# Optimization experiments

Hardware: AMD Instinct MI355X
Metric: run time of the kernel (lower is better)

## Reference

```python
import jax, jax.numpy as jnp
import numpy as np
import math

B, T, S = 32, 512, 256          # batch, tgt_len (prediction_length), src_len (encoder tokens)
PD, ED = 1, 768                 # pred_dim, encoder_dim
D, H, L, FF = 256, 8, 4, 1024   # d_model, nhead, num_layers, dim_feedforward
HD = D // H
NEG = -1e9
EPS = 1e-5


def _pos_encoding(seq_len, d_model):
    pos = jnp.arange(seq_len, dtype=jnp.float32)[:, None]
    div = jnp.exp(jnp.arange(0, d_model, 2, dtype=jnp.float32) * (-math.log(10000.0) / d_model))
    pe = jnp.zeros((seq_len, d_model), jnp.float32)
    pe = pe.at[:, 0::2].set(jnp.sin(pos * div))
    pe = pe.at[:, 1::2].set(jnp.cos(pos * div))
    return pe


def _ln(x, g, b):
    m = jnp.mean(x, -1, keepdims=True)
    v = jnp.mean((x - m) ** 2, -1, keepdims=True)
    return (x - m) * jax.lax.rsqrt(v + EPS) * g + b


def _mha(xq, xkv, Wq, bq, Wk, bk, Wv, bv, Wo, bo, mask):
    b, t, d = xq.shape
    s = xkv.shape[1]
    Q = (xq @ Wq + bq).reshape(b, t, H, HD).transpose(0, 2, 1, 3)   # bhtd
    K = (xkv @ Wk + bk).reshape(b, s, H, HD).transpose(0, 2, 1, 3)  # bhsd
    V = (xkv @ Wv + bv).reshape(b, s, H, HD).transpose(0, 2, 1, 3)
    scores = jnp.einsum('bhtd,bhsd->bhts', Q, K) * (HD ** -0.5)
    if mask is not None:
        scores = scores + mask
    w = jax.nn.softmax(scores, axis=-1)
    o = jnp.einsum('bhts,bhsd->bhtd', w, V).transpose(0, 2, 1, 3).reshape(b, t, d)
    return o @ Wo + bo


def _forward(tgt, memory, W_emb, b_emb, W_enc, b_enc,
             Wq_s, bq_s, Wk_s, bk_s, Wv_s, bv_s, Wo_s, bo_s,
             Wq_c, bq_c, Wk_c, bk_c, Wv_c, bv_c, Wo_c, bo_c,
             g1, be1, g2, be2, g3, be3, Wf1, bf1, Wf2, bf2,
             Wp1, bp1, Wp2, bp2):
    t = tgt.shape[1]
    x = tgt @ W_emb + b_emb + _pos_encoding(t, D)          # (B,T,D)
    mem = memory @ W_enc + b_enc                           # (B,S,D)
    causal = jnp.triu(jnp.full((t, t), NEG, jnp.float32), k=1)
    for i in range(L):
        sa = _mha(x, x, Wq_s[i], bq_s[i], Wk_s[i], bk_s[i], Wv_s[i], bv_s[i], Wo_s[i], bo_s[i], causal)
        x = _ln(x + sa, g1[i], be1[i])
        ca = _mha(x, mem, Wq_c[i], bq_c[i], Wk_c[i], bk_c[i], Wv_c[i], bv_c[i], Wo_c[i], bo_c[i], None)
        x = _ln(x + ca, g2[i], be2[i])
        ff = jax.nn.gelu(x @ Wf1[i] + bf1[i], approximate=False) @ Wf2[i] + bf2[i]
        x = _ln(x + ff, g3[i], be3[i])
    h = jax.nn.gelu(x @ Wp1 + bp1, approximate=False)
    return h @ Wp2 + bp2                                   # (B,T,PD)


def setup_inputs() -> dict:
    key = jax.random.key(0)
    keys = iter(jax.random.split(key, 40))
    def rn(shape, scale=0.05):
        return jax.random.normal(next(keys), shape, jnp.float32) * scale
    z = jnp.zeros
    inp = {
        'tgt': jax.random.normal(next(keys), (B, T, PD), jnp.float32),
        'memory': jax.random.normal(next(keys), (B, S, ED), jnp.float32),
        'W_emb': rn((PD, D)), 'b_emb': z((D,)),
        'W_enc': rn((ED, D)), 'b_enc': z((D,)),
        'Wq_s': rn((L, D, D)), 'bq_s': z((L, D)),
        'Wk_s': rn((L, D, D)), 'bk_s': z((L, D)),
        'Wv_s': rn((L, D, D)), 'bv_s': z((L, D)),
        'Wo_s': rn((L, D, D)), 'bo_s': z((L, D)),
        'Wq_c': rn((L, D, D)), 'bq_c': z((L, D)),
        'Wk_c': rn((L, D, D)), 'bk_c': z((L, D)),
        'Wv_c': rn((L, D, D)), 'bv_c': z((L, D)),
        'Wo_c': rn((L, D, D)), 'bo_c': z((L, D)),
        'g1': jnp.ones((L, D)), 'be1': z((L, D)),
        'g2': jnp.ones((L, D)), 'be2': z((L, D)),
        'g3': jnp.ones((L, D)), 'be3': z((L, D)),
        'Wf1': rn((L, D, FF)), 'bf1': z((L, FF)),
        'Wf2': rn((L, FF, D)), 'bf2': z((L, D)),
        'Wp1': rn((D, D // 2)), 'bp1': z((D // 2,)),
        'Wp2': rn((D // 2, PD), 0.01), 'bp2': jnp.full((PD,), 0.1, jnp.float32),
    }
    return inp


def reference(tgt, memory, W_emb, b_emb, W_enc, b_enc,
              Wq_s, bq_s, Wk_s, bk_s, Wv_s, bv_s, Wo_s, bo_s,
              Wq_c, bq_c, Wk_c, bk_c, Wv_c, bv_c, Wo_c, bo_c,
              g1, be1, g2, be2, g3, be3, Wf1, bf1, Wf2, bf2,
              Wp1, bp1, Wp2, bp2):
    return _forward(tgt, memory, W_emb, b_emb, W_enc, b_enc,
                    Wq_s, bq_s, Wk_s, bk_s, Wv_s, bv_s, Wo_s, bo_s,
                    Wq_c, bq_c, Wk_c, bk_c, Wv_c, bv_c, Wo_c, bo_c,
                    g1, be1, g2, be2, g3, be3, Wf1, bf1, Wf2, bf2,
                    Wp1, bp1, Wp2, bp2)
```

## Files before the change

kernel.cpp:

```cpp
#include <hip/hip_runtime.h>
#include <math.h>

#define B_  32
#define T_  512
#define S_  256
#define D_  256
#define H_  8
#define HD_ 32
#define FF_ 1024
#define ED_ 768
#define L_  4
#define BT_ (B_*T_)
#define BS_ (B_*S_)

typedef __bf16 bf16x8_t __attribute__((ext_vector_type(8)));
typedef __bf16 bf16x4_t __attribute__((ext_vector_type(4)));
typedef float  f32x4_t  __attribute__((ext_vector_type(4)));

__device__ __forceinline__ float gelu_f(float v) {
  return 0.5f * v * (1.f + erff(v * 0.7071067811865476f));
}

__device__ __forceinline__ void gl16(const __bf16* gsrc, __bf16* ldst) {
  __builtin_amdgcn_global_load_lds(
      (const __attribute__((address_space(1))) unsigned int*)gsrc,
      (__attribute__((address_space(3))) unsigned int*)ldst, 16, 0, 0);
}

__global__ __launch_bounds__(256)
void embed_kernel(const float* __restrict__ tgt, const float* __restrict__ Wemb,
                  const float* __restrict__ bemb, float* __restrict__ x,
                  __bf16* __restrict__ xbf) {
  int i = blockIdx.x * 256 + threadIdx.x;
  int d  = i & (D_ - 1);
  int bt = i >> 8;
  int t  = bt & (T_ - 1);
  int p  = d >> 1;
  float div = expf((float)(2 * p) * (-9.210340371976184f / (float)D_));
  float arg = (float)t * div;
  float pe = (d & 1) ? cosf(arg) : sinf(arg);
  float v = tgt[bt] * Wemb[d] + bemb[d] + pe;
  x[i] = v;
  xbf[i] = (__bf16)v;
}

__global__ __launch_bounds__(256)
void cvt_bf16_kernel(const float* __restrict__ in, __bf16* __restrict__ out) {
  int i = (blockIdx.x * 256 + threadIdx.x) * 4;
  float4 v = *(const float4*)(in + i);
  bf16x4_t o;
  o[0] = (__bf16)v.x; o[1] = (__bf16)v.y; o[2] = (__bf16)v.z; o[3] = (__bf16)v.w;
  *(bf16x4_t*)(out + i) = o;
}

struct TD { const float* src; size_t dst; int K, N, nb; size_t lstride; };
struct TDs { TD d[12]; };

__global__ __launch_bounds__(256)
void transpose_cvt_kernel(TDs a, __bf16* __restrict__ wt) {
  __shared__ float tile[32][33];
  TD t = a.d[blockIdx.y];
  const int kt = t.K >> 5, nt = t.N >> 5;
  const int per = kt * nt, tot = per * t.nb;
  const int id = blockIdx.x;
  if (id >= tot) return;
  const int b = id / per;
  const int r2 = id - b * per;
  const int kti = r2 / nt;
  const int nti = r2 - kti * nt;
  const int c = threadIdx.x & 31, r0 = threadIdx.x >> 5;
  const float* src = t.src + (size_t)b * t.K * t.N;
  __bf16* dst = wt + t.dst + (size_t)b * t.lstride;
#pragma unroll
  for (int j = 0; j < 4; ++j) {
    int rr = r0 + j * 8;
    tile[rr][c] = src[(size_t)(kti * 32 + rr) * t.N + nti * 32 + c];
  }
  __syncthreads();
#pragma unroll
  for (int j = 0; j < 4; ++j) {
    int rr = r0 + j * 8;
    dst[(size_t)(nti * 32 + rr) * t.K + kti * 32 + c] = (__bf16)tile[c][rr];
  }
}

__global__ __launch_bounds__(256)
void bias_concat_kernel(const float* __restrict__ bq_s, const float* __restrict__ bk_s,
                        const float* __restrict__ bv_s, const float* __restrict__ bk_c,
                        const float* __restrict__ bv_c, float* __restrict__ dst) {
  int idx = blockIdx.x * 256 + threadIdx.x;
  if (idx >= 5120) return;
  if (idx < 3072) {
    int l = idx / 768, c = idx - l * 768;
    float v = (c < 256) ? bq_s[l * 256 + c]
            : (c < 512) ? bk_s[l * 256 + c - 256]
                        : bv_s[l * 256 + c - 512];
    dst[idx] = v;
  } else {
    int j = idx - 3072;
    int l = j / 512, c = j - l * 512;
    float v = (c < 256) ? bk_c[l * 256 + c] : bv_c[l * 256 + c - 256];
    dst[idx] = v;
  }
}

template<int ACT, int OBF>
__global__ __launch_bounds__(256, 3)
void gemm_bf(const __bf16* __restrict__ A, const __bf16* __restrict__ Bt,
             const float* __restrict__ bias, void* __restrict__ Cv,
             int N, int K, int nN, int ppx) {
  __shared__ __bf16 As[128 * 64];
  __shared__ __bf16 Bs[64 * 64];
  const int tid = threadIdx.x, lane = tid & 63, wv = tid >> 6;
  const int wm = (wv & 1) * 64, wn = (wv >> 1) * 32;
  const int ln15 = lane & 15, kgrp = lane >> 4;
  const int xcd = blockIdx.x & 7, j = blockIdx.x >> 3;
  const int bm = (xcd * ppx + j / nN) * 128;
  const int bn = (j % nN) * 64;

  const int r8 = lane >> 3;
  const int scol = (lane & 7) ^ r8;
  const __bf16* a_g = A  + (size_t)(bm + wv * 32 + r8) * K + scol * 8;
  const __bf16* b_g = Bt + (size_t)(bn + wv * 16 + r8) * K + scol * 8;
  __bf16* a_l = As + wv * 2048;
  __bf16* b_l = Bs + wv * 1024;

  const int xk0 = kgrp ^ (ln15 & 7);
  const int xk1 = (4 + kgrp) ^ (ln15 & 7);

  f32x4_t acc[4][2];
#pragma unroll
  for (int mi = 0; mi < 4; ++mi)
#pragma unroll
    for (int ni = 0; ni < 2; ++ni) acc[mi][ni] = (f32x4_t){0.f, 0.f, 0.f, 0.f};

  for (int k0 = 0; k0 < K; k0 += 64) {
    gl16(a_g + k0,                a_l);
    gl16(a_g + k0 + (size_t)8*K,  a_l + 512);
    gl16(a_g + k0 + (size_t)16*K, a_l + 1024);
    gl16(a_g + k0 + (size_t)24*K, a_l + 1536);
    gl16(b_g + k0,                b_l);
    gl16(b_g + k0 + (size_t)8*K,  b_l + 512);
    __syncthreads();

#pragma unroll
    for (int kk = 0; kk < 2; ++kk) {
      const int xk = kk ? xk1 : xk0;
      bf16x8_t b0 = *(const bf16x8_t*)(Bs + ((wn + ln15) * 8 + xk) * 8);
      bf16x8_t b1 = *(const bf16x8_t*)(Bs + ((wn + 16 + ln15) * 8 + xk) * 8);
#pragma unroll
      for (int mi = 0; mi < 4; ++mi) {
        bf16x8_t af = *(const bf16x8_t*)(As + ((wm + mi * 16 + ln15) * 8 + xk) * 8);
        acc[mi][0] = __builtin_amdgcn_mfma_f32_16x16x32_bf16(af, b0, acc[mi][0], 0, 0, 0);
        acc[mi][1] = __builtin_amdgcn_mfma_f32_16x16x32_bf16(af, b1, acc[mi][1], 0, 0, 0);
      }
    }
    __syncthreads();
  }

#pragma unroll
  for (int mi = 0; mi < 4; ++mi) {
#pragma unroll
    for (int ni = 0; ni < 2; ++ni) {
      const int ocol = bn + wn + ni * 16 + ln15;
      const float bv = bias[ocol];
      const int orow0 = bm + wm + mi * 16 + kgrp * 4;
#pragma unroll
      for (int r = 0; r < 4; ++r) {
        float o = acc[mi][ni][r] + bv;
        if (ACT == 1) o = gelu_f(o);
        if (OBF) ((__bf16*)Cv)[(size_t)(orow0 + r) * N + ocol] = (__bf16)o;
        else     ((float*)Cv)[(size_t)(orow0 + r) * N + ocol] = o;
      }
    }
  }
}

template<int ACT, int OBF>
__global__ __launch_bounds__(256, 3)
void gemm_bf2(const __bf16* __restrict__ A, const __bf16* __restrict__ Bt,
              const float* __restrict__ bias, void* __restrict__ Cv,
              int N, int K, int nN, int ppx) {
  __shared__ __bf16 As[128 * 64];
  __shared__ __bf16 Bs[128 * 64];
  const int tid = threadIdx.x, lane = tid & 63, wv = tid >> 6;
  const int wm = (wv & 1) * 64, wn = (wv >> 1) * 64;
  const int ln15 = lane & 15, kgrp = lane >> 4;
  const int xcd = blockIdx.x & 7, j = blockIdx.x >> 3;
  const int bm = (xcd * ppx + j / nN) * 128;
  const int bn = (j % nN) * 128;

  const int r8 = lane >> 3;
  const int scol = (lane & 7) ^ r8;
  const __bf16* a_g = A  + (size_t)(bm + wv * 32 + r8) * K + scol * 8;
  const __bf16* b_g = Bt + (size_t)(bn + wv * 32 + r8) * K + scol * 8;
  __bf16* a_l = As + wv * 2048;
  __bf16* b_l = Bs + wv * 2048;

  const int xk0 = kgrp ^ (ln15 & 7);
  const int xk1 = (4 + kgrp) ^ (ln15 & 7);

  f32x4_t acc[4][4];
#pragma unroll
  for (int mi = 0; mi < 4; ++mi)
#pragma unroll
    for (int ni = 0; ni < 4; ++ni) acc[mi][ni] = (f32x4_t){0.f, 0.f, 0.f, 0.f};

  for (int k0 = 0; k0 < K; k0 += 64) {
    gl16(a_g + k0,                a_l);
    gl16(a_g + k0 + (size_t)8*K,  a_l + 512);
    gl16(a_g + k0 + (size_t)16*K, a_l + 1024);
    gl16(a_g + k0 + (size_t)24*K, a_l + 1536);
    gl16(b_g + k0,                b_l);
    gl16(b_g + k0 + (size_t)8*K,  b_l + 512);
    gl16(b_g + k0 + (size_t)16*K, b_l + 1024);
    gl16(b_g + k0 + (size_t)24*K, b_l + 1536);
    __syncthreads();

#pragma unroll
    for (int kk = 0; kk < 2; ++kk) {
      const int xk = kk ? xk1 : xk0;
      bf16x8_t bfr[4];
#pragma unroll
      for (int ni = 0; ni < 4; ++ni)
        bfr[ni] = *(const bf16x8_t*)(Bs + ((wn + ni * 16 + ln15) * 8 + xk) * 8);
#pragma unroll
      for (int mi = 0; mi < 4; ++mi) {
        bf16x8_t af = *(const bf16x8_t*)(As + ((wm + mi * 16 + ln15) * 8 + xk) * 8);
#pragma unroll
        for (int ni = 0; ni < 4; ++ni)
          acc[mi][ni] = __builtin_amdgcn_mfma_f32_16x16x32_bf16(af, bfr[ni], acc[mi][ni], 0, 0, 0);
      }
    }
    __syncthreads();
  }

#pragma unroll
  for (int mi = 0; mi < 4; ++mi) {
#pragma unroll
    for (int ni = 0; ni < 4; ++ni) {
      const int ocol = bn + wn + ni * 16 + ln15;
      const float bv = bias[ocol];
      const int orow0 = bm + wm + mi * 16 + kgrp * 4;
#pragma unroll
      for (int r = 0; r < 4; ++r) {
        float o = acc[mi][ni][r] + bv;
        if (ACT == 1) o = gelu_f(o);
        if (OBF) ((__bf16*)Cv)[(size_t)(orow0 + r) * N + ocol] = (__bf16)o;
        else     ((float*)Cv)[(size_t)(orow0 + r) * N + ocol] = o;
      }
    }
  }
}

template<bool CAUSAL>
__global__ __launch_bounds__(256)
void attn_mfma(const __bf16* __restrict__ Q, const __bf16* __restrict__ K,
               const __bf16* __restrict__ V, __bf16* __restrict__ O,
               int KVROWS, int qs, int ks) {
  const int b = blockIdx.x >> 3, h = blockIdx.x & 7;
  const int qt = blockIdx.y;
  const int tid = threadIdx.x, lane = tid & 63, wv = tid >> 6;
  const int ln15 = lane & 15, kgrp = lane >> 4, kgrp8 = kgrp * 8;

  __shared__ __bf16 K_lds[64][36];
  __shared__ __bf16 Vt_lds[32][72];
  __shared__ __bf16 P_lds[4][16][72];

  const int q_glob = qt * 64 + wv * 16 + ln15;
  const bf16x8_t qfrag = *(const bf16x8_t*)(Q + (size_t)(b * T_ + q_glob) * qs + h * HD_ + kgrp8);

  const int s_r = tid >> 2, s_c8 = (tid & 3) * 8;
  const __bf16* Kb = K + (size_t)(b * KVROWS + s_r) * ks + h * HD_ + s_c8;
  const __bf16* Vb = V + (size_t)(b * KVROWS + s_r) * ks + h * HD_ + s_c8;

  f32x4_t o0 = (f32x4_t){0.f,0.f,0.f,0.f}, o1 = (f32x4_t){0.f,0.f,0.f,0.f};
  float m = -3.0e38f, l = 0.f;
  const float SCALE = 0.17677669529663689f;
  const int slim = CAUSAL ? (qt + 1) * 64 : KVROWS;

  for (int s0 = 0; s0 < slim; s0 += 64) {
    *(bf16x8_t*)&K_lds[s_r][s_c8] = *(const bf16x8_t*)(Kb + (size_t)s0 * ks);
    bf16x8_t vv = *(const bf16x8_t*)(Vb + (size_t)s0 * ks);
#pragma unroll
    for (int jj = 0; jj < 8; ++jj) Vt_lds[s_c8 + jj][s_r] = vv[jj];
    __syncthreads();

    f32x4_t sa[4];
#pragma unroll
    for (int c = 0; c < 4; ++c) {
      bf16x8_t kf = *(const bf16x8_t*)&K_lds[c * 16 + ln15][kgrp8];
      sa[c] = __builtin_amdgcn_mfma_f32_16x16x32_bf16(kf, qfrag, (f32x4_t){0.f,0.f,0.f,0.f}, 0, 0, 0);
    }
    float v[16];
#pragma unroll
    for (int c = 0; c < 4; ++c)
#pragma unroll
      for (int r = 0; r < 4; ++r) {
        float s = sa[c][r] * SCALE;
        if (CAUSAL && (s0 + c * 16 + kgrp * 4 + r) > q_glob) s += -1e9f;
        v[c * 4 + r] = s;
      }
    float tmax = v[0];
#pragma unroll
    for (int r = 1; r < 16; ++r) tmax = fmaxf(tmax, v[r]);
    tmax = fmaxf(tmax, __shfl_xor(tmax, 16));
    tmax = fmaxf(tmax, __shfl_xor(tmax, 32));
    float mnew = fmaxf(m, tmax);
    float corr = __expf(m - mnew);

    float lsum = 0.f;
#pragma unroll
    for (int c = 0; c < 4; ++c) {
      bf16x4_t pc;
#pragma unroll
      for (int r = 0; r < 4; ++r) {
        float e = __expf(v[c * 4 + r] - mnew);
        lsum += e;
        pc[r] = (__bf16)e;
      }
      *(bf16x4_t*)&P_lds[wv][ln15][c * 16 + kgrp * 4] = pc;
    }
    lsum += __shfl_xor(lsum, 16);
    lsum += __shfl_xor(lsum, 32);
    l = l * corr + lsum;
    m = mnew;

    const float c0 = __shfl(corr, kgrp * 4 + 0);
    const float c1 = __shfl(corr, kgrp * 4 + 1);
    const float c2 = __shfl(corr, kgrp * 4 + 2);
    const float c3 = __shfl(corr, kgrp * 4 + 3);
    o0[0] *= c0; o0[1] *= c1; o0[2] *= c2; o0[3] *= c3;
    o1[0] *= c0; o1[1] *= c1; o1[2] *= c2; o1[3] *= c3;

    bf16x8_t pLo = *(const bf16x8_t*)&P_lds[wv][ln15][kgrp8];
    bf16x8_t pHi = *(const bf16x8_t*)&P_lds[wv][ln15][32 + kgrp8];
    bf16x8_t v0l = *(const bf16x8_t*)&Vt_lds[ln15][kgrp8];
    bf16x8_t v0h = *(const bf16x8_t*)&Vt_lds[ln15][32 + kgrp8];
    bf16x8_t v1l = *(const bf16x8_t*)&Vt_lds[16 + ln15][kgrp8];
    bf16x8_t v1h = *(const bf16x8_t*)&Vt_lds[16 + ln15][32 + kgrp8];
    o0 = __builtin_amdgcn_mfma_f32_16x16x32_bf16(pLo, v0l, o0, 0, 0, 0);
    o0 = __builtin_amdgcn_mfma_f32_16x16x32_bf16(pHi, v0h, o0, 0, 0, 0);
    o1 = __builtin_amdgcn_mfma_f32_16x16x32_bf16(pLo, v1l, o1, 0, 0, 0);
    o1 = __builtin_amdgcn_mfma_f32_16x16x32_bf16(pHi, v1h, o1, 0, 0, 0);
    __syncthreads();
  }

  const float inv = 1.f / l;
  const float i0 = __shfl(inv, kgrp * 4 + 0);
  const float i1 = __shfl(inv, kgrp * 4 + 1);
  const float i2 = __shfl(inv, kgrp * 4 + 2);
  const float i3 = __shfl(inv, kgrp * 4 + 3);
  __bf16* Op = O + (size_t)(b * T_ + qt * 64 + wv * 16 + kgrp * 4) * D_ + h * HD_;
  Op[0 * D_ + ln15] = (__bf16)(o0[0] * i0);  Op[0 * D_ + 16 + ln15] = (__bf16)(o1[0] * i0);
  Op[1 * D_ + ln15] = (__bf16)(o0[1] * i1);  Op[1 * D_ + 16 + ln15] = (__bf16)(o1[1] * i1);
  Op[2 * D_ + ln15] = (__bf16)(o0[2] * i2);  Op[2 * D_ + 16 + ln15] = (__bf16)(o1[2] * i2);
  Op[3 * D_ + ln15] = (__bf16)(o0[3] * i3);  Op[3 * D_ + 16 + ln15] = (__bf16)(o1[3] * i3);
}

__global__ __launch_bounds__(256)
void add_ln_kernel(float* __restrict__ x, __bf16* __restrict__ xbf,
                   const __bf16* __restrict__ y,
                   const float* __restrict__ g, const float* __restrict__ bta) {
  const int row = blockIdx.x * 4 + (threadIdx.x >> 6);
  const int lane = threadIdx.x & 63;
  const size_t base = (size_t)row * D_ + lane * 4;
  float4 xv = *(const float4*)&x[base];
  bf16x4_t yv = *(const bf16x4_t*)&y[base];
  float v0 = xv.x + (float)yv[0], v1 = xv.y + (float)yv[1];
  float v2 = xv.z + (float)yv[2], v3 = xv.w + (float)yv[3];
  float sum = v0 + v1 + v2 + v3;
  float sq  = v0 * v0 + v1 * v1 + v2 * v2 + v3 * v3;
#pragma unroll
  for (int off = 32; off; off >>= 1) {
    sum += __shfl_xor(sum, off);
    sq  += __shfl_xor(sq, off);
  }
  float mean = sum * (1.f / D_);
  float var  = sq * (1.f / D_) - mean * mean;
  float rstd = rsqrtf(fmaxf(var, 0.f) + 1e-5f);
  const int c = lane * 4;
  float4 gv = *(const float4*)&g[c];
  float4 bv = *(const float4*)&bta[c];
  float4 ov;
  ov.x = (v0 - mean) * rstd * gv.x + bv.x;
  ov.y = (v1 - mean) * rstd * gv.y + bv.y;
  ov.z = (v2 - mean) * rstd * gv.z + bv.z;
  ov.w = (v3 - mean) * rstd * gv.w + bv.w;
  *(float4*)&x[base] = ov;
  bf16x4_t ob;
  ob[0] = (__bf16)ov.x; ob[1] = (__bf16)ov.y; ob[2] = (__bf16)ov.z; ob[3] = (__bf16)ov.w;
  *(bf16x4_t*)&xbf[base] = ob;
}

__global__ __launch_bounds__(256)
void head2_kernel(const float* __restrict__ hb, const float* __restrict__ w,
                  const float* __restrict__ bias, float* __restrict__ out) {
  const int row = blockIdx.x * 4 + (threadIdx.x >> 6);
  const int lane = threadIdx.x & 63;
  float a = hb[(size_t)row * 128 + lane] * w[lane]
          + hb[(size_t)row * 128 + 64 + lane] * w[64 + lane];
#pragma unroll
  for (int off = 32; off; off >>= 1) a += __shfl_xor(a, off);
  if (lane == 0) out[row] = a + bias[0];
}

extern "C" void kernel_launch(void* const* d_in, const int* in_sizes, int n_in,
                              void* d_out, int out_size, void* d_ws, size_t ws_size,
                              hipStream_t stream) {
  const float* tgt    = (const float*)d_in[0];
  const float* memory = (const float*)d_in[1];
  const float* W_emb  = (const float*)d_in[2];
  const float* b_emb  = (const float*)d_in[3];
  const float* W_enc  = (const float*)d_in[4];
  const float* b_enc  = (const float*)d_in[5];
  const float* Wq_s = (const float*)d_in[6];  const float* bq_s = (const float*)d_in[7];
  const float* Wk_s = (const float*)d_in[8];  const float* bk_s = (const float*)d_in[9];
  const float* Wv_s = (const float*)d_in[10]; const float* bv_s = (const float*)d_in[11];
  const float* Wo_s = (const float*)d_in[12]; const float* bo_s = (const float*)d_in[13];
  const float* Wq_c = (const float*)d_in[14]; const float* bq_c = (const float*)d_in[15];
  const float* Wk_c = (const float*)d_in[16]; const float* bk_c = (const float*)d_in[17];
  const float* Wv_c = (const float*)d_in[18]; const float* bv_c = (const float*)d_in[19];
  const float* Wo_c = (const float*)d_in[20]; const float* bo_c = (const float*)d_in[21];
  const float* g1  = (const float*)d_in[22]; const float* be1 = (const float*)d_in[23];
  const float* g2  = (const float*)d_in[24]; const float* be2 = (const float*)d_in[25];
  const float* g3  = (const float*)d_in[26]; const float* be3 = (const float*)d_in[27];
  const float* Wf1 = (const float*)d_in[28]; const float* bf1 = (const float*)d_in[29];
  const float* Wf2 = (const float*)d_in[30]; const float* bf2 = (const float*)d_in[31];
  const float* Wp1 = (const float*)d_in[32]; const float* bp1 = (const float*)d_in[33];
  const float* Wp2 = (const float*)d_in[34]; const float* bp2 = (const float*)d_in[35];

  float*  x    = (float*)d_ws;
  float*  yf   = x + (size_t)BT_ * D_;
  __bf16* ybf  = (__bf16*)yf;
  __bf16* xbf  = (__bf16*)(yf + (size_t)BT_ * D_);
  __bf16* membf= xbf + (size_t)BT_ * D_;
  __bf16* qkv  = membf + (size_t)BS_ * D_;
  __bf16* ext  = qkv + (size_t)BT_ * 768;
  __bf16* ao   = ext + (size_t)4194304;
  __bf16* wt   = ao + (size_t)BT_ * D_;
  float*  bcat = (float*)(wt + 4423680);
  __bf16* memb = qkv;
  __bf16* qc   = qkv;
  __bf16* kvc  = qkv + (size_t)BT_ * D_;
  __bf16* ff   = qkv;

  const size_t o_enc  = 0;
  const size_t o_qkv  = 196608;
  const size_t o_qcw  = 983040;
  const size_t o_kvw  = 1245184;
  const size_t o_os   = 1769472;
  const size_t o_oc   = 2031616;
  const size_t o_f1   = 2293760;
  const size_t o_f2   = 3342336;
  const size_t o_p1   = 4390912;

  TDs td;
  td.d[0]  = {W_enc, o_enc,           ED_, D_,  1, 0};
  td.d[1]  = {Wq_s,  o_qkv + 0,       D_,  D_,  L_, 196608};
  td.d[2]  = {Wk_s,  o_qkv + 65536,   D_,  D_,  L_, 196608};
  td.d[3]  = {Wv_s,  o_qkv + 131072,  D_,  D_,  L_, 196608};
  td.d[4]  = {Wq_c,  o_qcw,           D_,  D_,  L_, 65536};
  td.d[5]  = {Wk_c,  o_kvw + 0,       D_,  D_,  L_, 131072};
  td.d[6]  = {Wv_c,  o_kvw + 65536,   D_,  D_,  L_, 131072};
  td.d[7]  = {Wo_s,  o_os,            D_,  D_,  L_, 65536};
  td.d[8]  = {Wo_c,  o_oc,            D_,  D_,  L_, 65536};
  td.d[9]  = {Wf1,   o_f1,            D_,  FF_, L_, 262144};
  td.d[10] = {Wf2,   o_f2,            FF_, D_,  L_, 262144};
  td.d[11] = {Wp1,   o_p1,            D_,  128, 1, 0};

  dim3 blk(256);
  cvt_bf16_kernel<<<BS_ * ED_ / 1024, blk, 0, stream>>>(memory, memb);
  transpose_cvt_kernel<<<dim3(1024, 12), blk, 0, stream>>>(td, wt);
  bias_concat_kernel<<<20, blk, 0, stream>>>(bq_s, bk_s, bv_s, bk_c, bv_c, bcat);
  embed_kernel<<<BT_ * D_ / 256, blk, 0, stream>>>(tgt, W_emb, b_emb, x, xbf);

  const float* bqkv = bcat;
  const float* bkv  = bcat + 3072;
  const dim3 gA(B_ * H_, T_ / 64);

  gemm_bf<0,1><<<64 * 4, blk, 0, stream>>>(memb, wt + o_enc, b_enc, membf, D_, ED_, 4, 8);

  for (int i = 0; i < L_; ++i) {
    gemm_bf2<0,1><<<128 * 6, blk, 0, stream>>>(xbf, wt + o_qkv + (size_t)i * 196608, bqkv + i * 768, qkv, 768, D_, 6, 16);
    attn_mfma<true><<<gA, blk, 0, stream>>>(qkv, qkv + 256, qkv + 512, ao, T_, 768, 768);
    gemm_bf<0,1><<<128 * 4, blk, 0, stream>>>(ao, wt + o_os + (size_t)i * 65536, bo_s + i * D_, ybf, D_, D_, 4, 16);
    add_ln_kernel<<<BT_ / 4, blk, 0, stream>>>(x, xbf, ybf, g1 + i * D_, be1 + i * D_);
    gemm_bf<0,1><<<128 * 4, blk, 0, stream>>>(xbf, wt + o_qcw + (size_t)i * 65536, bq_c + i * D_, qc, D_, D_, 4, 16);
    gemm_bf<0,1><<<64 * 8, blk, 0, stream>>>(membf, wt + o_kvw + (size_t)i * 131072, bkv + i * 512, kvc, 512, D_, 8, 8);
    attn_mfma<false><<<gA, blk, 0, stream>>>(qc, kvc, kvc + 256, ao, S_, 256, 512);
    gemm_bf<0,1><<<128 * 4, blk, 0, stream>>>(ao, wt + o_oc + (size_t)i * 65536, bo_c + i * D_, ybf, D_, D_, 4, 16);
    add_ln_kernel<<<BT_ / 4, blk, 0, stream>>>(x, xbf, ybf, g2 + i * D_, be2 + i * D_);
    gemm_bf2<1,1><<<128 * 8, blk, 0, stream>>>(xbf, wt + o_f1 + (size_t)i * 262144, bf1 + i * FF_, ff, FF_, D_, 8, 16);
    gemm_bf<0,1><<<128 * 4, blk, 0, stream>>>(ff, wt + o_f2 + (size_t)i * 262144, bf2 + i * D_, ybf, D_, FF_, 4, 16);
    add_ln_kernel<<<BT_ / 4, blk, 0, stream>>>(x, xbf, ybf, g3 + i * D_, be3 + i * D_);
  }
  gemm_bf<1,0><<<128 * 2, blk, 0, stream>>>(xbf, wt + o_p1, bp1, yf, 128, D_, 2, 16);
  head2_kernel<<<BT_ / 4, blk, 0, stream>>>(yf, Wp2, bp2, (float*)d_out);
}
```

Baseline: 710.9 us.

## Fuse output/FF2 GEMMs with residual LayerNorm and batch cross-attn KV projections

Adds a gemm_ln kernel in which each 512-thread block computes a full 64x256 output row tile, then adds bias and residual and applies LayerNorm in the epilogue, with row statistics reduced through shared memory. This replaces the separate GEMM plus add_ln_kernel pairs and removes the bf16 intermediate round trip and three launches per layer. The cross-attention K/V projections for all four layers are also hoisted into one wide GEMM before the loop, since memory does not change across layers. The trade-offs are fewer blocks (256) with a large shared-memory tile, which may hurt occupancy, plus a reworked workspace layout.

```diff
diff --git a/kernel.cpp b/kernel.cpp
--- a/kernel.cpp
+++ b/kernel.cpp
@@ -253,6 +253,114 @@
   }
 }
 
+__global__ __launch_bounds__(512)
+void gemm_ln(const __bf16* __restrict__ A, const __bf16* __restrict__ Bt,
+             const float* __restrict__ bias, const float* __restrict__ g,
+             const float* __restrict__ bta, float* __restrict__ x,
+             __bf16* __restrict__ xbf, int K, int ppx) {
+  __shared__ __bf16 As[64 * 64];
+  __shared__ __bf16 Bs[256 * 64];
+  __shared__ float red[64][8];
+  const int tid = threadIdx.x, lane = tid & 63, wv = tid >> 6;
+  const int wm = (wv >> 2) * 32, wn = (wv & 3) * 64;
+  const int ln15 = lane & 15, kgrp = lane >> 4;
+  const int xcd = blockIdx.x & 7, j = blockIdx.x >> 3;
+  const int bm = (xcd * ppx + j) * 64;
+
+  const int sr = tid >> 3;
+  const int sch = (tid & 7) ^ (sr & 7);
+  const __bf16* a_g = A  + (size_t)(bm + sr) * K + sch * 8;
+  const __bf16* b_g = Bt + (size_t)sr * K + sch * 8;
+  __bf16* a_l = As + wv * 512;
+  __bf16* b_l = Bs + wv * 512;
+
+  const int xk0 = kgrp ^ (ln15 & 7);
+  const int xk1 = (4 + kgrp) ^ (ln15 & 7);
+
+  f32x4_t acc[2][4];
+#pragma unroll
+  for (int mi = 0; mi < 2; ++mi)
+#pragma unroll
+    for (int ni = 0; ni < 4; ++ni) acc[mi][ni] = (f32x4_t){0.f, 0.f, 0.f, 0.f};
+
+  for (int k0 = 0; k0 < K; k0 += 64) {
+    gl16(a_g + k0,                 a_l);
+    gl16(b_g + k0,                 b_l);
+    gl16(b_g + k0 + (size_t)64*K,  b_l + 4096);
+    gl16(b_g + k0 + (size_t)128*K, b_l + 8192);
+    gl16(b_g + k0 + (size_t)192*K, b_l + 12288);
+    __syncthreads();
+
+#pragma unroll
+    for (int kk = 0; kk < 2; ++kk) {
+      const int xk = kk ? xk1 : xk0;
+      bf16x8_t bfr[4];
+#pragma unroll
+      for (int ni = 0; ni < 4; ++ni)
+        bfr[ni] = *(const bf16x8_t*)(Bs + ((wn + ni * 16 + ln15) * 8 + xk) * 8);
+#pragma unroll
+      for (int mi = 0; mi < 2; ++mi) {
+        bf16x8_t af = *(const bf16x8_t*)(As + ((wm + mi * 16 + ln15) * 8 + xk) * 8);
+#pragma unroll
+        for (int ni = 0; ni < 4; ++ni)
+          acc[mi][ni] = __builtin_amdgcn_mfma_f32_16x16x32_bf16(af, bfr[ni], acc[mi][ni], 0, 0, 0);
+      }
+    }
+    __syncthreads();
+  }
+
+  const int c0 = wn + ln15;
+  float bs[4], gg[4], bb[4];
+#pragma unroll
+  for (int ni = 0; ni < 4; ++ni) {
+    bs[ni] = bias[c0 + ni * 16];
+    gg[ni] = g[c0 + ni * 16];
+    bb[ni] = bta[c0 + ni * 16];
+  }
+  float v[2][4][4];
+#pragma unroll
+  for (int mi = 0; mi < 2; ++mi) {
+#pragma unroll
+    for (int r = 0; r < 4; ++r) {
+      const int row = bm + wm + mi * 16 + kgrp * 4 + r;
+      float s = 0.f, q = 0.f;
+#pragma unroll
+      for (int ni = 0; ni < 4; ++ni) {
+        float t = acc[mi][ni][r] + bs[ni] + x[(size_t)row * 256 + c0 + ni * 16];
+        v[mi][ni][r] = t; s += t; q += t * t;
+      }
+      s += __shfl_xor(s, 1); s += __shfl_xor(s, 2);
+      s += __shfl_xor(s, 4); s += __shfl_xor(s, 8);
+      q += __shfl_xor(q, 1); q += __shfl_xor(q, 2);
+      q += __shfl_xor(q, 4); q += __shfl_xor(q, 8);
+      if (ln15 == 0) {
+        red[wm + mi * 16 + kgrp * 4 + r][(wv & 3) * 2 + 0] = s;
+        red[wm + mi * 16 + kgrp * 4 + r][(wv & 3) * 2 + 1] = q;
+      }
+    }
+  }
+  __syncthreads();
+#pragma unroll
+  for (int mi = 0; mi < 2; ++mi) {
+#pragma unroll
+    for (int r = 0; r < 4; ++r) {
+      const int rl = wm + mi * 16 + kgrp * 4 + r;
+      const int row = bm + rl;
+      const float ms = red[rl][0] + red[rl][2] + red[rl][4] + red[rl][6];
+      const float mq = red[rl][1] + red[rl][3] + red[rl][5] + red[rl][7];
+      const float mean = ms * (1.f / 256.f);
+      const float var  = mq * (1.f / 256.f) - mean * mean;
+      const float rstd = rsqrtf(fmaxf(var, 0.f) + 1e-5f);
+#pragma unroll
+      for (int ni = 0; ni < 4; ++ni) {
+        float o = (v[mi][ni][r] - mean) * rstd * gg[ni] + bb[ni];
+        x[(size_t)row * 256 + c0 + ni * 16] = o;
+        xbf[(size_t)row * 256 + c0 + ni * 16] = (__bf16)o;
+      }
+    }
+  }
+}
+
 template<bool CAUSAL>
 __global__ __launch_bounds__(256)
 void attn_mfma(const __bf16* __restrict__ Q, const __bf16* __restrict__ K,
@@ -356,41 +464,6 @@
   Op[1 * D_ + ln15] = (__bf16)(o0[1] * i1);  Op[1 * D_ + 16 + ln15] = (__bf16)(o1[1] * i1);
   Op[2 * D_ + ln15] = (__bf16)(o0[2] * i2);  Op[2 * D_ + 16 + ln15] = (__bf16)(o1[2] * i2);
   Op[3 * D_ + ln15] = (__bf16)(o0[3] * i3);  Op[3 * D_ + 16 + ln15] = (__bf16)(o1[3] * i3);
-}
-
-__global__ __launch_bounds__(256)
-void add_ln_kernel(float* __restrict__ x, __bf16* __restrict__ xbf,
-                   const __bf16* __restrict__ y,
-                   const float* __restrict__ g, const float* __restrict__ bta) {
-  const int row = blockIdx.x * 4 + (threadIdx.x >> 6);
-  const int lane = threadIdx.x & 63;
-  const size_t base = (size_t)row * D_ + lane * 4;
-  float4 xv = *(const float4*)&x[base];
-  bf16x4_t yv = *(const bf16x4_t*)&y[base];
-  float v0 = xv.x + (float)yv[0], v1 = xv.y + (float)yv[1];
-  float v2 = xv.z + (float)yv[2], v3 = xv.w + (float)yv[3];
-  float sum = v0 + v1 + v2 + v3;
-  float sq  = v0 * v0 + v1 * v1 + v2 * v2 + v3 * v3;
-#pragma unroll
-  for (int off = 32; off; off >>= 1) {
-    sum += __shfl_xor(sum, off);
-    sq  += __shfl_xor(sq, off);
-  }
-  float mean = sum * (1.f / D_);
-  float var  = sq * (1.f / D_) - mean * mean;
-  float rstd = rsqrtf(fmaxf(var, 0.f) + 1e-5f);
-  const int c = lane * 4;
-  float4 gv = *(const float4*)&g[c];
-  float4 bv = *(const float4*)&bta[c];
-  float4 ov;
-  ov.x = (v0 - mean) * rstd * gv.x + bv.x;
-  ov.y = (v1 - mean) * rstd * gv.y + bv.y;
-  ov.z = (v2 - mean) * rstd * gv.z + bv.z;
-  ov.w = (v3 - mean) * rstd * gv.w + bv.w;
-  *(float4*)&x[base] = ov;
-  bf16x4_t ob;
-  ob[0] = (__bf16)ov.x; ob[1] = (__bf16)ov.y; ob[2] = (__bf16)ov.z; ob[3] = (__bf16)ov.w;
-  *(bf16x4_t*)&xbf[base] = ob;
 }
 
 __global__ __launch_bounds__(256)
@@ -430,20 +503,19 @@
   const float* Wp1 = (const float*)d_in[32]; const float* bp1 = (const float*)d_in[33];
   const float* Wp2 = (const float*)d_in[34]; const float* bp2 = (const float*)d_in[35];
 
-  float*  x    = (float*)d_ws;
-  float*  yf   = x + (size_t)BT_ * D_;
-  __bf16* ybf  = (__bf16*)yf;
-  __bf16* xbf  = (__bf16*)(yf + (size_t)BT_ * D_);
-  __bf16* membf= xbf + (size_t)BT_ * D_;
-  __bf16* qkv  = membf + (size_t)BS_ * D_;
-  __bf16* ext  = qkv + (size_t)BT_ * 768;
-  __bf16* ao   = ext + (size_t)4194304;
-  __bf16* wt   = ao + (size_t)BT_ * D_;
-  float*  bcat = (float*)(wt + 4423680);
-  __bf16* memb = qkv;
-  __bf16* qc   = qkv;
-  __bf16* kvc  = qkv + (size_t)BT_ * D_;
-  __bf16* ff   = qkv;
+  float*  x     = (float*)d_ws;
+  __bf16* xbf   = (__bf16*)(x + (size_t)4194304);
+  __bf16* membf = xbf + (size_t)4194304;
+  __bf16* wt    = (__bf16*)((float*)membf + 1048576);
+  float*  bcat  = (float*)(wt + 4423680);
+  __bf16* kvall = (__bf16*)(bcat + 8192);
+  __bf16* scr   = kvall + (size_t)16777216;
+  __bf16* ao    = scr + (size_t)16777216;
+  __bf16* memb = scr;
+  __bf16* qkv  = scr;
+  __bf16* qc   = scr;
+  __bf16* ff   = scr;
+  float*  hbuf = (float*)ao;
 
   const size_t o_enc  = 0;
   const size_t o_qkv  = 196608;
@@ -480,21 +552,21 @@
   const dim3 gA(B_ * H_, T_ / 64);
 
   gemm_bf<0,1><<<64 * 4, blk, 0, stream>>>(memb, wt + o_enc, b_enc, membf, D_, ED_, 4, 8);
+  gemm_bf2<0,1><<<64 * 16, blk, 0, stream>>>(membf, wt + o_kvw, bkv, kvall, 2048, D_, 16, 8);
 
   for (int i = 0; i < L_; ++i) {
     gemm_bf2<0,1><<<128 * 6, blk, 0, stream>>>(xbf, wt + o_qkv + (size_t)i * 196608, bqkv + i * 768, qkv, 768, D_, 6, 16);
     attn_mfma<true><<<gA, blk, 0, stream>>>(qkv, qkv + 256, qkv + 512, ao, T_, 768, 768);
-    gemm_bf<0,1><<<128 * 4, blk, 0, stream>>>(ao, wt + o_os + (size_t)i * 65536, bo_s + i * D_, ybf, D_, D_, 4, 16);
-    add_ln_kernel<<<BT_ / 4, blk, 0, stream>>>(x, xbf, ybf, g1 + i * D_, be1 + i * D_);
+    gemm_ln<<<256, dim3(512), 0, stream>>>(ao, wt + o_os + (size_t)i * 65536, bo_s + i * D_,
+                                           g1 + i * D_, be1 + i * D_, x, xbf, D_, 32);
     gemm_bf<0,1><<<128 * 4, blk, 0, stream>>>(xbf, wt + o_qcw + (size_t)i * 65536, bq_c + i * D_, qc, D_, D_, 4, 16);
-    gemm_bf<0,1><<<64 * 8, blk, 0, stream>>>(membf, wt + o_kvw + (size_t)i * 131072, bkv + i * 512, kvc, 512, D_, 8, 8);
-    attn_mfma<false><<<gA, blk, 0, stream>>>(qc, kvc, kvc + 256, ao, S_, 256, 512);
-    gemm_bf<0,1><<<128 * 4, blk, 0, stream>>>(ao, wt + o_oc + (size_t)i * 65536, bo_c + i * D_, ybf, D_, D_, 4, 16);
-    add_ln_kernel<<<BT_ / 4, blk, 0, stream>>>(x, xbf, ybf, g2 + i * D_, be2 + i * D_);
+    attn_mfma<false><<<gA, blk, 0, stream>>>(qc, kvall + i * 512, kvall + i * 512 + 256, ao, S_, 256, 2048);
+    gemm_ln<<<256, dim3(512), 0, stream>>>(ao, wt + o_oc + (size_t)i * 65536, bo_c + i * D_,
+                                           g2 + i * D_, be2 + i * D_, x, xbf, D_, 32);
     gemm_bf2<1,1><<<128 * 8, blk, 0, stream>>>(xbf, wt + o_f1 + (size_t)i * 262144, bf1 + i * FF_, ff, FF_, D_, 8, 16);
-    gemm_bf<0,1><<<128 * 4, blk, 0, stream>>>(ff, wt + o_f2 + (size_t)i * 262144, bf2 + i * D_, ybf, D_, FF_, 4, 16);
-    add_ln_kernel<<<BT_ / 4, blk, 0, stream>>>(x, xbf, ybf, g3 + i * D_, be3 + i * D_);
-  }
-  gemm_bf<1,0><<<128 * 2, blk, 0, stream>>>(xbf, wt + o_p1, bp1, yf, 128, D_, 2, 16);
-  head2_kernel<<<BT_ / 4, blk, 0, stream>>>(yf, Wp2, bp2, (float*)d_out);
-}
+    gemm_ln<<<256, dim3(512), 0, stream>>>(ff, wt + o_f2 + (size_t)i * 262144, bf2 + i * D_,
+                                           g3 + i * D_, be3 + i * D_, x, xbf, FF_, 32);
+  }
+  gemm_bf<1,0><<<128 * 2, blk, 0, stream>>>(xbf, wt + o_p1, bp1, hbuf, 128, D_, 2, 16);
+  head2_kernel<<<BT_ / 4, blk, 0, stream>>>(hbuf, Wp2, bp2, (float*)d_out);
+}
```

New measurement: 697.4 us. Within noise of the previous version (-1.9%).
